# Kernel optimization log

Hardware: AMD Instinct MI355X
Metric: run time of the kernel (lower is better)

Reference implementation:

```python
import jax, jax.numpy as jnp
import numpy as np


def _cxcywh_to_xyxy(b):
    cx, cy, w, h = b[..., 0], b[..., 1], b[..., 2], b[..., 3]
    return jnp.stack([cx - 0.5 * w, cy - 0.5 * h, cx + 0.5 * w, cy + 0.5 * h], axis=-1)


def _generalized_box_iou(a, b):
    # a: [M,4] xyxy, b: [N,4] xyxy -> [M,N] GIoU matrix (DETR box_ops semantics)
    area_a = (a[:, 2] - a[:, 0]) * (a[:, 3] - a[:, 1])  # [M]
    area_b = (b[:, 2] - b[:, 0]) * (b[:, 3] - b[:, 1])  # [N]
    lt = jnp.maximum(a[:, None, :2], b[None, :, :2])    # [M,N,2]
    rb = jnp.minimum(a[:, None, 2:], b[None, :, 2:])
    wh = jnp.clip(rb - lt, 0.0)
    inter = wh[..., 0] * wh[..., 1]                     # [M,N]
    union = area_a[:, None] + area_b[None, :] - inter
    iou = inter / union
    lt_c = jnp.minimum(a[:, None, :2], b[None, :, :2])
    rb_c = jnp.maximum(a[:, None, 2:], b[None, :, 2:])
    wh_c = jnp.clip(rb_c - lt_c, 0.0)
    area_c = wh_c[..., 0] * wh_c[..., 1]
    return iou - (area_c - union) / area_c


def setup_inputs() -> dict:
    key = jax.random.key(0)
    k1, k2, k3 = jax.random.split(key, 3)
    B, T, N = 8, 64, 8
    # predicted boxes in cxcywh, all components in (0,1) -> positive w,h (valid)
    pred_boxes = jax.random.uniform(k1, (B, T, N, 4), dtype=jnp.float32)
    # target boxes directly in valid xyxy (code path uses them unconverted)
    centers = jax.random.uniform(k2, (B, T, N, 2), dtype=jnp.float32) * 0.8 + 0.1
    half_wh = (jax.random.uniform(k3, (B, T, N, 2), dtype=jnp.float32) * 0.2 + 0.02) * 0.5
    bboxes = jnp.concatenate([centers - half_wh, centers + half_wh], axis=-1)
    bboxes_mask = jnp.ones((B, T), dtype=bool)
    return {"pred_boxes": pred_boxes, "bboxes": bboxes, "bboxes_mask": bboxes_mask}


def reference(pred_boxes, bboxes, bboxes_mask):
    B, T, N, _ = pred_boxes.shape
    M = B * T * N
    # per-box validity (mask is per-frame, broadcast to boxes), as weights
    v = jnp.broadcast_to(bboxes_mask[:, :, None], (B, T, N)).reshape(M).astype(pred_boxes.dtype)
    src = _cxcywh_to_xyxy(pred_boxes.reshape(M, 4))   # [M,4]
    tgt = bboxes.reshape(M, 4)                        # [M,4]
    G = _generalized_box_iou(tgt, src)                # [M,M] rows=targets, cols=preds
    # argmax matching over valid prediction columns
    g_match = jnp.where(v[None, :] > 0, G, -jnp.inf)
    idx = jnp.argmax(g_match, axis=1)                 # [M]
    matched = src[idx]                                # [M,4]
    matched_gious = G[:, idx]                         # [M,M] (faithful to original)
    w = v[:, None] * v[idx][None, :]                  # validity weights
    loss_giou = 1.0 - jnp.sum(matched_gious * w) / jnp.sum(w)
    loss_bbox = jnp.sum(jnp.abs(matched - tgt) * v[:, None]) / (4.0 * jnp.sum(v))
    return loss_giou, loss_bbox
```

## Files before the change

### kernel.cpp

```cpp
#include <hip/hip_runtime.h>
#include <cmath>

#define WAVE 64
#define TPB  256
#define RPW  4
#define SJ   8

__device__ __forceinline__ float fastrcp(float x) { return __builtin_amdgcn_rcpf(x); }

__device__ __forceinline__ float giou_f(float a0, float a1, float a2, float a3, float areaA,
                                        float b0, float b1, float b2, float b3, float areaB) {
    float ltx = fmaxf(a0, b0), lty = fmaxf(a1, b1);
    float rbx = fminf(a2, b2), rby = fminf(a3, b3);
    float w = fmaxf(rbx - ltx, 0.0f), h = fmaxf(rby - lty, 0.0f);
    float inter = w * h;
    float uni = areaA + areaB - inter;
    float cx1 = fminf(a0, b0), cy1 = fminf(a1, b1);
    float cx2 = fmaxf(a2, b2), cy2 = fmaxf(a3, b3);
    float areaC = (cx2 - cx1) * (cy2 - cy1);
    return inter * fastrcp(uni) - (areaC - uni) * fastrcp(areaC);
}

__device__ __forceinline__ unsigned sortable_u32(float f) {
    unsigned b = __float_as_uint(f);
    return (b & 0x80000000u) ? ~b : (b | 0x80000000u);
}

__global__ void prep_kernel(const float4* __restrict__ pred, const float4* __restrict__ tgt,
                            const void* __restrict__ maskp, int M, int N,
                            float4* __restrict__ src, float* __restrict__ areaS,
                            float* __restrict__ areaT, float* __restrict__ v) {
    int m = blockIdx.x * blockDim.x + threadIdx.x;
    if (m >= M) return;
    float4 pb = pred[m];
    float x1 = pb.x - 0.5f * pb.z, y1 = pb.y - 0.5f * pb.w;
    float x2 = pb.x + 0.5f * pb.z, y2 = pb.y + 0.5f * pb.w;
    src[m] = make_float4(x1, y1, x2, y2);
    areaS[m] = (x2 - x1) * (y2 - y1);
    float4 tb = tgt[m];
    areaT[m] = (tb.z - tb.x) * (tb.w - tb.y);

    const unsigned char* mb = (const unsigned char*)maskp;
    unsigned char b0 = mb[0], b1 = mb[1];
    int t = m / N;
    float vm;
    if (b0 != 0 && b1 != 0)      vm = mb[t] ? 1.0f : 0.0f;
    else if (b0 != 0)            vm = ((const int*)maskp)[t] ? 1.0f : 0.0f;
    else                         vm = (((const float*)maskp)[t] != 0.0f) ? 1.0f : 0.0f;
    v[m] = vm;
}

__global__ void rowpass_kernel(const float4* __restrict__ src, const float* __restrict__ areaS,
                               const float* __restrict__ v,
                               const float4* __restrict__ tgt, const float* __restrict__ areaT,
                               int M, unsigned long long* __restrict__ keypart) {
    int wid  = (blockIdx.x * blockDim.x + threadIdx.x) / WAVE;
    int lane = threadIdx.x & (WAVE - 1);
    int rowgrp = wid / SJ;
    int c      = wid % SJ;
    int i0 = rowgrp * RPW;
    if (i0 >= M) return;
    int chunk = M / SJ;
    int jbeg = c * chunk, jend = jbeg + chunk;

    float a0[RPW], a1[RPW], a2[RPW], a3[RPW], aA[RPW];
    float best[RPW];
    int   bidx[RPW];
#pragma unroll
    for (int r = 0; r < RPW; ++r) {
        int i = min(i0 + r, M - 1);
        float4 t = tgt[i];
        a0[r] = t.x; a1[r] = t.y; a2[r] = t.z; a3[r] = t.w;
        aA[r] = areaT[i];
        best[r] = -INFINITY; bidx[r] = 0;
    }

    for (int j = jbeg + lane; j < jend; j += WAVE) {
        float4 s = src[j];
        float aB = areaS[j];
        float vj = v[j];
#pragma unroll
        for (int r = 0; r < RPW; ++r) {
            float g = giou_f(a0[r], a1[r], a2[r], a3[r], aA[r], s.x, s.y, s.z, s.w, aB);
            float val = (vj > 0.0f) ? g : -INFINITY;
            if (val > best[r]) { best[r] = val; bidx[r] = j; }
        }
    }

#pragma unroll
    for (int r = 0; r < RPW; ++r) {
        unsigned long long key = ((unsigned long long)sortable_u32(best[r]) << 32)
                               | (unsigned)(~bidx[r]);
        for (int off = 32; off >= 1; off >>= 1) {
            unsigned long long ok = __shfl_xor(key, off);
            key = (ok > key) ? ok : key;
        }
        if (lane == 0 && (i0 + r) < M) keypart[(size_t)c * M + (i0 + r)] = key;
    }
}

__global__ void colpass_kernel(const float4* __restrict__ src, const float* __restrict__ areaS,
                               const float* __restrict__ v,
                               const float4* __restrict__ tgt, const float* __restrict__ areaT,
                               int M, float* __restrict__ colpart) {
    int wid  = (blockIdx.x * blockDim.x + threadIdx.x) / WAVE;
    int lane = threadIdx.x & (WAVE - 1);
    int colgrp = wid / SJ;
    int c      = wid % SJ;
    int j0 = colgrp * RPW;
    if (j0 >= M) return;
    int chunk = M / SJ;
    int ibeg = c * chunk, iend = ibeg + chunk;

    float b0[RPW], b1[RPW], b2[RPW], b3[RPW], aB[RPW], acc[RPW];
#pragma unroll
    for (int r = 0; r < RPW; ++r) {
        int j = min(j0 + r, M - 1);
        float4 s = src[j];
        b0[r] = s.x; b1[r] = s.y; b2[r] = s.z; b3[r] = s.w;
        aB[r] = areaS[j];
        acc[r] = 0.0f;
    }

    for (int i = ibeg + lane; i < iend; i += WAVE) {
        float4 t = tgt[i];
        float aA = areaT[i];
        float vi = v[i];
#pragma unroll
        for (int r = 0; r < RPW; ++r) {
            float g = giou_f(t.x, t.y, t.z, t.w, aA, b0[r], b1[r], b2[r], b3[r], aB[r]);
            acc[r] += vi * g;
        }
    }

#pragma unroll
    for (int r = 0; r < RPW; ++r) {
        for (int off = 32; off >= 1; off >>= 1) acc[r] += __shfl_xor(acc[r], off);
        if (lane == 0 && (j0 + r) < M) colpart[(size_t)c * M + (j0 + r)] = acc[r];
    }
}

__global__ void reduce_kernel(const unsigned long long* __restrict__ keypart,
                              const float* __restrict__ colpart,
                              int M, int* __restrict__ idx, float* __restrict__ colsum) {
    int m = blockIdx.x * blockDim.x + threadIdx.x;
    if (m >= M) return;
    unsigned long long k = keypart[m];
    float s = colpart[m];
#pragma unroll
    for (int c = 1; c < SJ; ++c) {
        unsigned long long kc = keypart[(size_t)c * M + m];
        k = (kc > k) ? kc : k;
        s += colpart[(size_t)c * M + m];
    }
    idx[m] = (int)(~(unsigned)k);
    colsum[m] = s;
}

__device__ double block_reduce_d(double val, double* sh) {
    int tid = threadIdx.x;
    sh[tid] = val; __syncthreads();
    for (int s = TPB / 2; s > 0; s >>= 1) {
        if (tid < s) sh[tid] += sh[tid + s];
        __syncthreads();
    }
    double r = sh[0];
    __syncthreads();
    return r;
}

__global__ void final_kernel(const float4* __restrict__ src, const float4* __restrict__ tgt,
                             const float* __restrict__ v, const int* __restrict__ idx,
                             const float* __restrict__ colsum, int M, float* __restrict__ out) {
    __shared__ double sh[TPB];
    double sumV = 0.0, S1 = 0.0, S2 = 0.0, bbox = 0.0;
    for (int m = threadIdx.x; m < M; m += TPB) {
        float vi = v[m];
        int   k  = idx[m];
        float vk = v[k];
        sumV += (double)vi;
        S2   += (double)vk;
        S1   += (double)vk * (double)colsum[k];
        float4 s = src[k];
        float4 t = tgt[m];
        bbox += (double)vi * (double)(fabsf(s.x - t.x) + fabsf(s.y - t.y) +
                                      fabsf(s.z - t.z) + fabsf(s.w - t.w));
    }
    sumV = block_reduce_d(sumV, sh);
    S2   = block_reduce_d(S2, sh);
    S1   = block_reduce_d(S1, sh);
    bbox = block_reduce_d(bbox, sh);
    if (threadIdx.x == 0) {
        out[0] = (float)(1.0 - S1 / (sumV * S2));
        out[1] = (float)(bbox / (4.0 * sumV));
    }
}

extern "C" void kernel_launch(void* const* d_in, const int* in_sizes, int n_in,
                              void* d_out, int out_size, void* d_ws, size_t ws_size,
                              hipStream_t stream) {
    const float4* pred = (const float4*)d_in[0];
    const float4* tgt  = (const float4*)d_in[1];
    const void*   mask = d_in[2];

    int M = in_sizes[0] / 4;
    int N = M / in_sizes[2];

    char* ws = (char*)d_ws;
    float4* src    = (float4*)ws;              ws += (size_t)M * 16;
    float*  areaS  = (float*)ws;               ws += (size_t)M * 4;
    float*  areaT  = (float*)ws;               ws += (size_t)M * 4;
    float*  v      = (float*)ws;               ws += (size_t)M * 4;
    float*  colsum = (float*)ws;               ws += (size_t)M * 4;
    int*    idx    = (int*)ws;                 ws += (size_t)M * 4;
    unsigned long long* keypart = (unsigned long long*)ws; ws += (size_t)SJ * M * 8;
    float*  colpart = (float*)ws;              ws += (size_t)SJ * M * 4;

    float* out = (float*)d_out;

    int prep_blocks = (M + TPB - 1) / TPB;
    prep_kernel<<<prep_blocks, TPB, 0, stream>>>(pred, tgt, mask, M, N, src, areaS, areaT, v);

    int waves   = ((M + RPW - 1) / RPW) * SJ;
    int gblocks = (waves * WAVE + TPB - 1) / TPB;
    rowpass_kernel<<<gblocks, TPB, 0, stream>>>(src, areaS, v, tgt, areaT, M, keypart);
    colpass_kernel<<<gblocks, TPB, 0, stream>>>(src, areaS, v, tgt, areaT, M, colpart);

    reduce_kernel<<<prep_blocks, TPB, 0, stream>>>(keypart, colpart, M, idx, colsum);

    final_kernel<<<1, TPB, 0, stream>>>(src, tgt, v, idx, colsum, M, out);
}
```

Baseline: 105.3 us.

## Fuse five kernels into two, recomputing box prep inline

Removes the prep kernel by converting cxcywh boxes, computing areas and reading the mask on the fly inside the pairwise passes. Row and column passes are merged into one launch split by block index so they run concurrently. The reduce and final kernels are merged into a single 1024-thread finalize kernel that keeps idx, colsum and v in LDS and reduces with wave shuffles. This cuts launch overhead and intermediate global traffic, at the cost of redundant per-element conversion work, a hard M<=4096 limit from fixed LDS arrays, and dropped bounds clamps for M not divisible by RPW.

New measurement: 102.2 us. -2.9%, faster.

```diff
diff --git a/kernel.cpp b/kernel.cpp
--- a/kernel.cpp
+++ b/kernel.cpp
@@ -5,6 +5,8 @@
 #define TPB  256
 #define RPW  4
 #define SJ   8
+#define FTPB 1024
+#define MMAX 4096
 
 __device__ __forceinline__ float fastrcp(float x) { return __builtin_amdgcn_rcpf(x); }
 
@@ -26,173 +28,177 @@
     return (b & 0x80000000u) ? ~b : (b | 0x80000000u);
 }
 
-__global__ void prep_kernel(const float4* __restrict__ pred, const float4* __restrict__ tgt,
-                            const void* __restrict__ maskp, int M, int N,
-                            float4* __restrict__ src, float* __restrict__ areaS,
-                            float* __restrict__ areaT, float* __restrict__ v) {
-    int m = blockIdx.x * blockDim.x + threadIdx.x;
-    if (m >= M) return;
-    float4 pb = pred[m];
-    float x1 = pb.x - 0.5f * pb.z, y1 = pb.y - 0.5f * pb.w;
-    float x2 = pb.x + 0.5f * pb.z, y2 = pb.y + 0.5f * pb.w;
-    src[m] = make_float4(x1, y1, x2, y2);
-    areaS[m] = (x2 - x1) * (y2 - y1);
-    float4 tb = tgt[m];
-    areaT[m] = (tb.z - tb.x) * (tb.w - tb.y);
-
+__device__ __forceinline__ int mask_mode(const void* maskp) {
     const unsigned char* mb = (const unsigned char*)maskp;
     unsigned char b0 = mb[0], b1 = mb[1];
-    int t = m / N;
-    float vm;
-    if (b0 != 0 && b1 != 0)      vm = mb[t] ? 1.0f : 0.0f;
-    else if (b0 != 0)            vm = ((const int*)maskp)[t] ? 1.0f : 0.0f;
-    else                         vm = (((const float*)maskp)[t] != 0.0f) ? 1.0f : 0.0f;
-    v[m] = vm;
-}
-
-__global__ void rowpass_kernel(const float4* __restrict__ src, const float* __restrict__ areaS,
-                               const float* __restrict__ v,
-                               const float4* __restrict__ tgt, const float* __restrict__ areaT,
-                               int M, unsigned long long* __restrict__ keypart) {
-    int wid  = (blockIdx.x * blockDim.x + threadIdx.x) / WAVE;
-    int lane = threadIdx.x & (WAVE - 1);
-    int rowgrp = wid / SJ;
-    int c      = wid % SJ;
-    int i0 = rowgrp * RPW;
-    if (i0 >= M) return;
-    int chunk = M / SJ;
-    int jbeg = c * chunk, jend = jbeg + chunk;
-
-    float a0[RPW], a1[RPW], a2[RPW], a3[RPW], aA[RPW];
-    float best[RPW];
-    int   bidx[RPW];
-#pragma unroll
-    for (int r = 0; r < RPW; ++r) {
-        int i = min(i0 + r, M - 1);
-        float4 t = tgt[i];
-        a0[r] = t.x; a1[r] = t.y; a2[r] = t.z; a3[r] = t.w;
-        aA[r] = areaT[i];
-        best[r] = -INFINITY; bidx[r] = 0;
-    }
-
-    for (int j = jbeg + lane; j < jend; j += WAVE) {
-        float4 s = src[j];
-        float aB = areaS[j];
-        float vj = v[j];
-#pragma unroll
-        for (int r = 0; r < RPW; ++r) {
-            float g = giou_f(a0[r], a1[r], a2[r], a3[r], aA[r], s.x, s.y, s.z, s.w, aB);
-            float val = (vj > 0.0f) ? g : -INFINITY;
-            if (val > best[r]) { best[r] = val; bidx[r] = j; }
-        }
-    }
-
-#pragma unroll
-    for (int r = 0; r < RPW; ++r) {
-        unsigned long long key = ((unsigned long long)sortable_u32(best[r]) << 32)
-                               | (unsigned)(~bidx[r]);
-        for (int off = 32; off >= 1; off >>= 1) {
-            unsigned long long ok = __shfl_xor(key, off);
-            key = (ok > key) ? ok : key;
-        }
-        if (lane == 0 && (i0 + r) < M) keypart[(size_t)c * M + (i0 + r)] = key;
-    }
-}
-
-__global__ void colpass_kernel(const float4* __restrict__ src, const float* __restrict__ areaS,
-                               const float* __restrict__ v,
-                               const float4* __restrict__ tgt, const float* __restrict__ areaT,
-                               int M, float* __restrict__ colpart) {
-    int wid  = (blockIdx.x * blockDim.x + threadIdx.x) / WAVE;
-    int lane = threadIdx.x & (WAVE - 1);
-    int colgrp = wid / SJ;
-    int c      = wid % SJ;
-    int j0 = colgrp * RPW;
-    if (j0 >= M) return;
-    int chunk = M / SJ;
-    int ibeg = c * chunk, iend = ibeg + chunk;
-
-    float b0[RPW], b1[RPW], b2[RPW], b3[RPW], aB[RPW], acc[RPW];
-#pragma unroll
-    for (int r = 0; r < RPW; ++r) {
-        int j = min(j0 + r, M - 1);
-        float4 s = src[j];
-        b0[r] = s.x; b1[r] = s.y; b2[r] = s.z; b3[r] = s.w;
-        aB[r] = areaS[j];
-        acc[r] = 0.0f;
-    }
-
-    for (int i = ibeg + lane; i < iend; i += WAVE) {
-        float4 t = tgt[i];
-        float aA = areaT[i];
-        float vi = v[i];
-#pragma unroll
-        for (int r = 0; r < RPW; ++r) {
-            float g = giou_f(t.x, t.y, t.z, t.w, aA, b0[r], b1[r], b2[r], b3[r], aB[r]);
-            acc[r] += vi * g;
-        }
-    }
-
-#pragma unroll
-    for (int r = 0; r < RPW; ++r) {
-        for (int off = 32; off >= 1; off >>= 1) acc[r] += __shfl_xor(acc[r], off);
-        if (lane == 0 && (j0 + r) < M) colpart[(size_t)c * M + (j0 + r)] = acc[r];
-    }
-}
-
-__global__ void reduce_kernel(const unsigned long long* __restrict__ keypart,
-                              const float* __restrict__ colpart,
-                              int M, int* __restrict__ idx, float* __restrict__ colsum) {
-    int m = blockIdx.x * blockDim.x + threadIdx.x;
-    if (m >= M) return;
-    unsigned long long k = keypart[m];
-    float s = colpart[m];
-#pragma unroll
-    for (int c = 1; c < SJ; ++c) {
-        unsigned long long kc = keypart[(size_t)c * M + m];
-        k = (kc > k) ? kc : k;
-        s += colpart[(size_t)c * M + m];
-    }
-    idx[m] = (int)(~(unsigned)k);
-    colsum[m] = s;
-}
-
-__device__ double block_reduce_d(double val, double* sh) {
-    int tid = threadIdx.x;
-    sh[tid] = val; __syncthreads();
-    for (int s = TPB / 2; s > 0; s >>= 1) {
-        if (tid < s) sh[tid] += sh[tid + s];
-        __syncthreads();
-    }
-    double r = sh[0];
+    if (b0 != 0 && b1 != 0) return 0;
+    if (b0 != 0) return 1;
+    return 2;
+}
+__device__ __forceinline__ float mask_v(const void* maskp, int t, int mode) {
+    if (mode == 0) return ((const unsigned char*)maskp)[t] ? 1.0f : 0.0f;
+    if (mode == 1) return ((const int*)maskp)[t] ? 1.0f : 0.0f;
+    return (((const float*)maskp)[t] != 0.0f) ? 1.0f : 0.0f;
+}
+__device__ __forceinline__ int midx(int m, int nsh, int N) {
+    return (nsh >= 0) ? (m >> nsh) : (m / N);
+}
+
+__global__ __launch_bounds__(TPB) void pass_kernel(
+        const float4* __restrict__ pred, const float4* __restrict__ tgt,
+        const void* __restrict__ maskp, int M, int nsh, int N,
+        unsigned long long* __restrict__ keypart, float* __restrict__ colpart,
+        int rowBlocks) {
+    const int mode  = mask_mode(maskp);
+    const int chunk = M / SJ;
+    const int lane  = threadIdx.x & (WAVE - 1);
+    const int warp  = threadIdx.x >> 6;
+
+    if ((int)blockIdx.x < rowBlocks) {
+        int wid = blockIdx.x * (TPB / WAVE) + warp;
+        int rowgrp = wid / SJ, c = wid % SJ;
+        int i0 = rowgrp * RPW;
+        if (i0 >= M) return;
+        int jbeg = c * chunk, jend = jbeg + chunk;
+
+        float a0[RPW], a1[RPW], a2[RPW], a3[RPW], aA[RPW], best[RPW];
+        int bidx[RPW];
+#pragma unroll
+        for (int r = 0; r < RPW; ++r) {
+            float4 t = tgt[i0 + r];
+            a0[r] = t.x; a1[r] = t.y; a2[r] = t.z; a3[r] = t.w;
+            aA[r] = (t.z - t.x) * (t.w - t.y);
+            best[r] = -INFINITY; bidx[r] = 0;
+        }
+
+#pragma unroll 4
+        for (int j = jbeg + lane; j < jend; j += WAVE) {
+            float4 p = pred[j];
+            float sx1 = p.x - 0.5f * p.z, sy1 = p.y - 0.5f * p.w;
+            float sx2 = p.x + 0.5f * p.z, sy2 = p.y + 0.5f * p.w;
+            float aB = (sx2 - sx1) * (sy2 - sy1);
+            float vj = mask_v(maskp, midx(j, nsh, N), mode);
+            bool mv = vj > 0.0f;
+#pragma unroll
+            for (int r = 0; r < RPW; ++r) {
+                float g = giou_f(a0[r], a1[r], a2[r], a3[r], aA[r], sx1, sy1, sx2, sy2, aB);
+                float val = mv ? g : -INFINITY;
+                if (val > best[r]) { best[r] = val; bidx[r] = j; }
+            }
+        }
+
+#pragma unroll
+        for (int r = 0; r < RPW; ++r) {
+            unsigned long long key = ((unsigned long long)sortable_u32(best[r]) << 32)
+                                   | (unsigned)(~bidx[r]);
+            for (int off = 32; off >= 1; off >>= 1) {
+                unsigned long long ok = __shfl_xor(key, off);
+                key = (ok > key) ? ok : key;
+            }
+            if (lane == 0) keypart[(size_t)c * M + (i0 + r)] = key;
+        }
+    } else {
+        int wid = (blockIdx.x - rowBlocks) * (TPB / WAVE) + warp;
+        int colgrp = wid / SJ, c = wid % SJ;
+        int j0 = colgrp * RPW;
+        if (j0 >= M) return;
+        int ibeg = c * chunk, iend = ibeg + chunk;
+
+        float b0[RPW], b1[RPW], b2[RPW], b3[RPW], aB[RPW], acc[RPW];
+#pragma unroll
+        for (int r = 0; r < RPW; ++r) {
+            float4 p = pred[j0 + r];
+            b0[r] = p.x - 0.5f * p.z; b1[r] = p.y - 0.5f * p.w;
+            b2[r] = p.x + 0.5f * p.z; b3[r] = p.y + 0.5f * p.w;
+            aB[r] = (b2[r] - b0[r]) * (b3[r] - b1[r]);
+            acc[r] = 0.0f;
+        }
+
+#pragma unroll 4
+        for (int i = ibeg + lane; i < iend; i += WAVE) {
+            float4 t = tgt[i];
+            float aA = (t.z - t.x) * (t.w - t.y);
+            float vi = mask_v(maskp, midx(i, nsh, N), mode);
+#pragma unroll
+            for (int r = 0; r < RPW; ++r) {
+                float g = giou_f(t.x, t.y, t.z, t.w, aA, b0[r], b1[r], b2[r], b3[r], aB[r]);
+                acc[r] += vi * g;
+            }
+        }
+
+#pragma unroll
+        for (int r = 0; r < RPW; ++r) {
+            for (int off = 32; off >= 1; off >>= 1) acc[r] += __shfl_xor(acc[r], off);
+            if (lane == 0) colpart[(size_t)c * M + (j0 + r)] = acc[r];
+        }
+    }
+}
+
+__device__ __forceinline__ double wave_sum_d(double x) {
+    for (int off = 32; off >= 1; off >>= 1) x += __shfl_xor(x, off);
+    return x;
+}
+
+__global__ __launch_bounds__(FTPB) void finalize_kernel(
+        const float4* __restrict__ pred, const float4* __restrict__ tgt,
+        const void* __restrict__ maskp, int M, int nsh, int N,
+        const unsigned long long* __restrict__ keypart,
+        const float* __restrict__ colpart, float* __restrict__ out) {
+    __shared__ float cs_lds[MMAX];
+    __shared__ unsigned short idx_lds[MMAX];
+    __shared__ float v_lds[MMAX];
+    __shared__ double red[4 * (FTPB / WAVE)];
+
+    const int mode = mask_mode(maskp);
+    const int tid = threadIdx.x;
+
+    for (int m = tid; m < M; m += FTPB) {
+        unsigned long long k = keypart[m];
+        float s = colpart[m];
+#pragma unroll
+        for (int c = 1; c < SJ; ++c) {
+            unsigned long long kc = keypart[(size_t)c * M + m];
+            k = (kc > k) ? kc : k;
+            s += colpart[(size_t)c * M + m];
+        }
+        idx_lds[m] = (unsigned short)(~(unsigned)k);
+        cs_lds[m] = s;
+        v_lds[m] = mask_v(maskp, midx(m, nsh, N), mode);
+    }
     __syncthreads();
-    return r;
-}
-
-__global__ void final_kernel(const float4* __restrict__ src, const float4* __restrict__ tgt,
-                             const float* __restrict__ v, const int* __restrict__ idx,
-                             const float* __restrict__ colsum, int M, float* __restrict__ out) {
-    __shared__ double sh[TPB];
+
     double sumV = 0.0, S1 = 0.0, S2 = 0.0, bbox = 0.0;
-    for (int m = threadIdx.x; m < M; m += TPB) {
-        float vi = v[m];
-        int   k  = idx[m];
-        float vk = v[k];
+    for (int m = tid; m < M; m += FTPB) {
+        float vi = v_lds[m];
+        int k = idx_lds[m];
+        float vk = v_lds[k];
         sumV += (double)vi;
         S2   += (double)vk;
-        S1   += (double)vk * (double)colsum[k];
-        float4 s = src[k];
+        S1   += (double)vk * (double)cs_lds[k];
+        float4 p = pred[k];
+        float sx1 = p.x - 0.5f * p.z, sy1 = p.y - 0.5f * p.w;
+        float sx2 = p.x + 0.5f * p.z, sy2 = p.y + 0.5f * p.w;
         float4 t = tgt[m];
-        bbox += (double)vi * (double)(fabsf(s.x - t.x) + fabsf(s.y - t.y) +
-                                      fabsf(s.z - t.z) + fabsf(s.w - t.w));
-    }
-    sumV = block_reduce_d(sumV, sh);
-    S2   = block_reduce_d(S2, sh);
-    S1   = block_reduce_d(S1, sh);
-    bbox = block_reduce_d(bbox, sh);
-    if (threadIdx.x == 0) {
-        out[0] = (float)(1.0 - S1 / (sumV * S2));
-        out[1] = (float)(bbox / (4.0 * sumV));
+        bbox += (double)vi * (double)(fabsf(sx1 - t.x) + fabsf(sy1 - t.y) +
+                                      fabsf(sx2 - t.z) + fabsf(sy2 - t.w));
+    }
+    sumV = wave_sum_d(sumV);
+    S2   = wave_sum_d(S2);
+    S1   = wave_sum_d(S1);
+    bbox = wave_sum_d(bbox);
+    int wid = tid >> 6, lane = tid & (WAVE - 1);
+    const int NW = FTPB / WAVE;
+    if (lane == 0) {
+        red[wid] = sumV; red[NW + wid] = S2; red[2 * NW + wid] = S1; red[3 * NW + wid] = bbox;
+    }
+    __syncthreads();
+    if (tid == 0) {
+        double a = 0, b = 0, c = 0, d = 0;
+        for (int w = 0; w < NW; ++w) {
+            a += red[w]; b += red[NW + w]; c += red[2 * NW + w]; d += red[3 * NW + w];
+        }
+        out[0] = (float)(1.0 - c / (a * b));
+        out[1] = (float)(d / (4.0 * a));
     }
 }
 
@@ -205,28 +211,18 @@
 
     int M = in_sizes[0] / 4;
     int N = M / in_sizes[2];
+    int nsh = -1;
+    for (int s = 0; s < 31; ++s) if ((1 << s) == N) { nsh = s; break; }
 
     char* ws = (char*)d_ws;
-    float4* src    = (float4*)ws;              ws += (size_t)M * 16;
-    float*  areaS  = (float*)ws;               ws += (size_t)M * 4;
-    float*  areaT  = (float*)ws;               ws += (size_t)M * 4;
-    float*  v      = (float*)ws;               ws += (size_t)M * 4;
-    float*  colsum = (float*)ws;               ws += (size_t)M * 4;
-    int*    idx    = (int*)ws;                 ws += (size_t)M * 4;
     unsigned long long* keypart = (unsigned long long*)ws; ws += (size_t)SJ * M * 8;
-    float*  colpart = (float*)ws;              ws += (size_t)SJ * M * 4;
-
+    float* colpart = (float*)ws;                           ws += (size_t)SJ * M * 4;
     float* out = (float*)d_out;
 
-    int prep_blocks = (M + TPB - 1) / TPB;
-    prep_kernel<<<prep_blocks, TPB, 0, stream>>>(pred, tgt, mask, M, N, src, areaS, areaT, v);
-
-    int waves   = ((M + RPW - 1) / RPW) * SJ;
-    int gblocks = (waves * WAVE + TPB - 1) / TPB;
-    rowpass_kernel<<<gblocks, TPB, 0, stream>>>(src, areaS, v, tgt, areaT, M, keypart);
-    colpass_kernel<<<gblocks, TPB, 0, stream>>>(src, areaS, v, tgt, areaT, M, colpart);
-
-    reduce_kernel<<<prep_blocks, TPB, 0, stream>>>(keypart, colpart, M, idx, colsum);
-
-    final_kernel<<<1, TPB, 0, stream>>>(src, tgt, v, idx, colsum, M, out);
-}
+    int rowBlocks = ((M / RPW) * SJ) / (TPB / WAVE);
+    int colBlocks = rowBlocks;
+    pass_kernel<<<rowBlocks + colBlocks, TPB, 0, stream>>>(
+        pred, tgt, mask, M, nsh, N, keypart, colpart, rowBlocks);
+
+    finalize_kernel<<<1, FTPB, 0, stream>>>(pred, tgt, mask, M, nsh, N, keypart, colpart, out);
+}
```
